# Optimization experiments

Hardware: AMD Instinct MI355X
Metric: run time of the kernel (lower is better)

The kernel has to match this reference:

```python
import jax, jax.numpy as jnp
import numpy as np

B, N_PER, D_IN, D_OUT, E_PER = 64, 256, 256, 128, 8192  # graphs, nodes/graph, in feat, out feat (=clusters K), edges/graph
EPS = 1e-12


def _sage(h, src, dst, W, b):
    # DenseSAGEConv (mean aggregator): h [n,Din], src/dst [E]
    agg = jnp.zeros_like(h).at[dst].add(h[src])                 # sum of in-neighbor messages
    deg = jnp.zeros((h.shape[0],), h.dtype).at[dst].add(1.0)
    agg = agg / jnp.maximum(deg, 1.0)[:, None]                  # mean aggregation
    z = jnp.concatenate([h, agg], axis=-1) @ W + b              # Linear(2*Din -> Dout)
    z = z / jnp.maximum(jnp.linalg.norm(z, axis=-1, keepdims=True), EPS)  # F.normalize(p=2)
    return jax.nn.relu(z)                                       # activation


def setup_inputs() -> dict:
    key = jax.random.key(0)
    ks = jax.random.split(key, 5)
    h = jax.random.normal(ks[0], (B, N_PER, D_IN), jnp.float32)
    edge_src = jax.random.randint(ks[1], (B, E_PER), 0, N_PER)
    edge_dst = jax.random.randint(ks[2], (B, E_PER), 0, N_PER)
    s = 1.0 / np.sqrt(2 * D_IN)
    W_feat = jax.random.uniform(ks[3], (2 * D_IN, D_OUT), jnp.float32, -s, s)
    b_feat = jnp.zeros((D_OUT,), jnp.float32)
    W_pool = jax.random.uniform(ks[4], (2 * D_IN, D_OUT), jnp.float32, -s, s)
    b_pool = jnp.zeros((D_OUT,), jnp.float32)
    return {"h": h, "edge_src": edge_src, "edge_dst": edge_dst,
            "W_feat": W_feat, "b_feat": b_feat, "W_pool": W_pool, "b_pool": b_pool}


def reference(h, edge_src, edge_dst, W_feat, b_feat, W_pool, b_pool):
    sage = jax.vmap(_sage, in_axes=(0, 0, 0, None, None))
    feat = sage(h, edge_src, edge_dst, W_feat, b_feat)                          # [B,n,K]
    assign = jax.nn.softmax(sage(h, edge_src, edge_dst, W_pool, b_pool), -1)    # [B,n,K]
    # h = assign^T @ feat, per graph (equivalent to block_diag(assign)^T @ stacked feat)
    h_pool = jnp.einsum('bnk,bnd->bkd', assign, feat).reshape(B * D_OUT, D_OUT)  # [B*K, Dout]
    # adj_new = S^T A S per graph; A[dst,src]=1 per edge -> sum_e outer(S[dst_e], S[src_e])
    s_dst = jnp.take_along_axis(assign, edge_dst[:, :, None], axis=1)           # [B,E,K]
    s_src = jnp.take_along_axis(assign, edge_src[:, :, None], axis=1)           # [B,E,K]
    blocks = jnp.einsum('bek,bel->bkl', s_dst, s_src)                           # [B,K,K]
    # cross-graph blocks are exactly zero in the batched graph -> block-diagonal dense adj
    adj_new = jax.scipy.linalg.block_diag(*blocks)                              # [B*K, B*K]
    return adj_new, h_pool
```

## Files before the change

### kernel.cpp

```cpp
#include <hip/hip_runtime.h>
#include <hip/hip_bf16.h>
#include <stdint.h>

#define BG 64
#define NP 256
#define DI 256
#define DO 128
#define EP 8192


typedef __attribute__((ext_vector_type(8))) short short8;
typedef __attribute__((ext_vector_type(4))) short short4v;
typedef __attribute__((ext_vector_type(4))) float float4v;

__device__ __forceinline__ int ldi(const void* p, size_t i, int i64) {
  return i64 ? (int)((const long long*)p)[i] : ((const int*)p)[i];
}

__device__ __forceinline__ short f2b(float x) {
  union { float f; unsigned u; } c; c.f = x;
  unsigned r = c.u + 0x7FFFu + ((c.u >> 16) & 1u);
  return (short)(r >> 16);
}
__device__ __forceinline__ float b2f(short b) {
  union { unsigned u; float f; } c; c.u = ((unsigned)(unsigned short)b) << 16;
  return c.f;
}

__device__ __forceinline__ int vote_i64(const void* esrc) {
  const uint32_t* ew = (const uint32_t*)esrc;
  int i64 = 1;
#pragma unroll
  for (int j = 0; j < 8; ++j)
    if (ew[2 * j + 1] != 0) i64 = 0;
  return i64;
}

__global__ __launch_bounds__(256) void k_scatter(const void* __restrict__ esrc,
                                                 const void* __restrict__ edst,
                                                 short* __restrict__ Abf,
                                                 float* __restrict__ deg) {
  __shared__ float Asl[64][256];
  int b = blockIdx.y, rq = blockIdx.x, t = threadIdx.x;
  float4* Az = (float4*)&Asl[0][0];
  for (int i = t; i < 64 * 256 / 4; i += 256) Az[i] = make_float4(0.f, 0.f, 0.f, 0.f);
  int i64 = vote_i64(esrc);
  __syncthreads();
  const size_t base = (size_t)b * EP;
  for (int e = t; e < EP; e += 256) {
    int si = ldi(esrc, base + e, i64) & (NP - 1);
    int di = ldi(edst, base + e, i64) & (NP - 1);
    if ((di >> 6) == rq) atomicAdd(&Asl[di & 63][si], 1.0f);
  }
  __syncthreads();
  int wv = t >> 6, ln = t & 63;
#pragma unroll
  for (int k = 0; k < 16; ++k) {
    int r = k * 4 + wv;
    float4 v = *(float4*)&Asl[r][ln * 4];
    int gr = rq * 64 + r;
    size_t o = ((size_t)b * NP + gr) * NP + ln * 4;
    short tmp[4] = { f2b(v.x), f2b(v.y), f2b(v.z), f2b(v.w) };
    *(short4v*)&Abf[o] = *(short4v*)tmp;
    float s = v.x + v.y + v.z + v.w;
    s += __shfl_xor(s, 1);  s += __shfl_xor(s, 2);  s += __shfl_xor(s, 4);
    s += __shfl_xor(s, 8);  s += __shfl_xor(s, 16); s += __shfl_xor(s, 32);
    if (ln == 0) deg[b * NP + gr] = s;
  }
}

__global__ __launch_bounds__(256) void k_htr(const float* __restrict__ h,
                                             short* __restrict__ hThi,
                                             short* __restrict__ hTlo) {
  __shared__ float T[64][65];
  int b = blockIdx.z, n0 = blockIdx.x * 64, f0 = blockIdx.y * 64;
  int t = threadIdx.x;
  int r = t >> 4, c4 = (t & 15) * 4;
#pragma unroll
  for (int i = 0; i < 4; ++i) {
    float4 v = *(const float4*)&h[((size_t)b * NP + n0 + i * 16 + r) * DI + f0 + c4];
    T[i * 16 + r][c4 + 0] = v.x; T[i * 16 + r][c4 + 1] = v.y;
    T[i * 16 + r][c4 + 2] = v.z; T[i * 16 + r][c4 + 3] = v.w;
  }
  __syncthreads();
#pragma unroll
  for (int i = 0; i < 4; ++i) {
    int f = i * 16 + r;
    short hi4[4], lo4[4];
#pragma unroll
    for (int j = 0; j < 4; ++j) {
      float x = T[c4 + j][f];
      short hb = f2b(x);
      hi4[j] = hb;
      lo4[j] = f2b(x - b2f(hb));
    }
    size_t o = ((size_t)b * DI + f0 + f) * NP + n0 + c4;
    *(short4v*)&hThi[o] = *(short4v*)hi4;
    *(short4v*)&hTlo[o] = *(short4v*)lo4;
  }
}

__global__ __launch_bounds__(256) void k_gemm_agg(const short* __restrict__ Abf,
                                                  const short* __restrict__ hThi,
                                                  const short* __restrict__ hTlo,
                                                  const float* __restrict__ deg,
                                                  float* __restrict__ agg) {
  int b = blockIdx.y, r0 = blockIdx.x * 32, t = threadIdx.x;
  int wave = t >> 6, lane = t & 63, rt = wave & 1, fh = wave >> 1;
  int m = lane & 15, q = lane >> 4;
  float4v acc[8];
#pragma unroll
  for (int i = 0; i < 8; ++i) acc[i] = (float4v){0.f, 0.f, 0.f, 0.f};
  const short* Ar = &Abf[((size_t)b * NP + r0 + rt * 16 + m) * NP];
  for (int kc = 0; kc < NP; kc += 32) {
    short8 af = *(const short8*)&Ar[kc + q * 8];
#pragma unroll
    for (int tt = 0; tt < 8; ++tt) {
      int f = fh * 128 + tt * 16 + m;
      short8 bh = *(const short8*)&hThi[((size_t)b * DI + f) * NP + kc + q * 8];
      short8 bl = *(const short8*)&hTlo[((size_t)b * DI + f) * NP + kc + q * 8];
      acc[tt] = __builtin_amdgcn_mfma_f32_16x16x32_bf16(af, bh, acc[tt], 0, 0, 0);
      acc[tt] = __builtin_amdgcn_mfma_f32_16x16x32_bf16(af, bl, acc[tt], 0, 0, 0);
    }
  }
#pragma unroll
  for (int reg = 0; reg < 4; ++reg) {
    int row = r0 + rt * 16 + q * 4 + reg;
    float sc = 1.0f / fmaxf(deg[b * NP + row], 1.0f);
#pragma unroll
    for (int tt = 0; tt < 8; ++tt)
      agg[((size_t)b * NP + row) * DI + fh * 128 + tt * 16 + m] = acc[tt][reg] * sc;
  }
}

__global__ __launch_bounds__(256) void k_wt(const float* __restrict__ Wf,
                                            const float* __restrict__ Wp,
                                            short* __restrict__ Wt) {
  __shared__ __align__(16) float T[32][132];
  int b = blockIdx.x;
  int head = b >> 4;
  int k0 = (b & 15) * 32;
  const float* W = head ? Wp : Wf;
  int t = threadIdx.x;
  {
    int k = t >> 3, fs = (t & 7) * 16;
    const float* src = &W[(size_t)(k0 + k) * DO + fs];
#pragma unroll
    for (int j = 0; j < 4; ++j)
      *(float4*)&T[k][fs + j * 4] = *(const float4*)(src + j * 4);
  }
  __syncthreads();
  int f = t & 127, kh = (t >> 7) * 16;
  __align__(16) short tmp[16];
#pragma unroll
  for (int i = 0; i < 16; ++i) tmp[i] = f2b(T[kh + i][f]);
  short* dst = &Wt[((size_t)head * DO + f) * 512 + k0 + kh];
  *(short8*)dst = *(short8*)&tmp[0];
  *(short8*)(dst + 8) = *(short8*)&tmp[8];
}

__global__ __launch_bounds__(256) void k_zepi_mfma(const float* __restrict__ h,
                                                   const float* __restrict__ agg,
                                                   const short* __restrict__ Wt,
                                                   const float* __restrict__ bfe,
                                                   const float* __restrict__ bpo,
                                                   short* __restrict__ FtH,
                                                   short* __restrict__ FtL,
                                                   short* __restrict__ PtH,
                                                   short* __restrict__ PtL) {
  __shared__ __align__(16) short Xs[32][40];
  __shared__ __align__(16) short TT[2][2][128][40];
  int r0 = blockIdx.x * 32;
  int t = threadIdx.x;
  int wave = t >> 6, lane = t & 63;
  int rt = wave & 1, ch = wave >> 1;
  int m = lane & 15, q = lane >> 4;
  float4v acc[8];
#pragma unroll
  for (int i = 0; i < 8; ++i) acc[i] = (float4v){0.f, 0.f, 0.f, 0.f};

  for (int kc = 0; kc < 2 * DI; kc += 32) {
    __syncthreads();
    {
      int r = t >> 3, k4 = (t & 7) * 4;
      const float* src = (kc < DI) ? &h[(size_t)(r0 + r) * DI + kc + k4]
                                   : &agg[(size_t)(r0 + r) * DI + (kc - DI) + k4];
      float4 v = *(const float4*)src;
      Xs[r][k4 + 0] = f2b(v.x); Xs[r][k4 + 1] = f2b(v.y);
      Xs[r][k4 + 2] = f2b(v.z); Xs[r][k4 + 3] = f2b(v.w);
    }
    __syncthreads();
    short8 afrag = *(const short8*)&Xs[rt * 16 + m][q * 8];
#pragma unroll
    for (int tt = 0; tt < 8; ++tt) {
      int n = ch * 128 + tt * 16 + m;
      short8 bfrag = *(const short8*)&Wt[(size_t)n * 512 + kc + q * 8];
      acc[tt] = __builtin_amdgcn_mfma_f32_16x16x32_bf16(afrag, bfrag, acc[tt], 0, 0, 0);
    }
  }

  const float* bp = ch ? bpo : bfe;
  float bias[8];
#pragma unroll
  for (int tt = 0; tt < 8; ++tt) bias[tt] = bp ? bp[tt * 16 + m] : 0.f;
#pragma unroll
  for (int reg = 0; reg < 4; ++reg) {
    int rloc = rt * 16 + q * 4 + reg;
    float z[8];
    float ss = 0.f;
#pragma unroll
    for (int tt = 0; tt < 8; ++tt) { z[tt] = acc[tt][reg] + bias[tt]; ss += z[tt] * z[tt]; }
    ss += __shfl_xor(ss, 1); ss += __shfl_xor(ss, 2);
    ss += __shfl_xor(ss, 4); ss += __shfl_xor(ss, 8);
    float inv = 1.0f / fmaxf(sqrtf(ss), 1e-12f);
    float v[8];
#pragma unroll
    for (int tt = 0; tt < 8; ++tt) v[tt] = fmaxf(z[tt] * inv, 0.f);
    if (ch == 1) {
      float mx = v[0];
#pragma unroll
      for (int tt = 1; tt < 8; ++tt) mx = fmaxf(mx, v[tt]);
      mx = fmaxf(mx, __shfl_xor(mx, 1)); mx = fmaxf(mx, __shfl_xor(mx, 2));
      mx = fmaxf(mx, __shfl_xor(mx, 4)); mx = fmaxf(mx, __shfl_xor(mx, 8));
      float e[8], s = 0.f;
#pragma unroll
      for (int tt = 0; tt < 8; ++tt) { e[tt] = __expf(v[tt] - mx); s += e[tt]; }
      s += __shfl_xor(s, 1); s += __shfl_xor(s, 2);
      s += __shfl_xor(s, 4); s += __shfl_xor(s, 8);
      float is = 1.0f / s;
#pragma unroll
      for (int tt = 0; tt < 8; ++tt) v[tt] = e[tt] * is;
    }
#pragma unroll
    for (int tt = 0; tt < 8; ++tt) {
      short hb = f2b(v[tt]);
      short lb = f2b(v[tt] - b2f(hb));
      TT[ch][0][tt * 16 + m][rloc] = hb;
      TT[ch][1][tt * 16 + m][rloc] = lb;
    }
  }
  __syncthreads();
  int b = r0 >> 8, nl = r0 & 255;
#pragma unroll
  for (int it = 0; it < 8; ++it) {
    int chunk = it * 256 + t;
    int c = chunk & 3, col = (chunk >> 2) & 127;
    int hl = (chunk >> 9) & 1, head = chunk >> 10;
    short* base = head ? (hl ? PtL : PtH) : (hl ? FtL : FtH);
    short* dst = &base[((size_t)b * DO + col) * NP + nl + c * 8];
    *(short8*)dst = *(const short8*)&TT[head][hl][col][c * 8];
  }
}

__global__ __launch_bounds__(256) void k_gemm_as(const short* __restrict__ Abf,
                                                 const short* __restrict__ PtH,
                                                 const short* __restrict__ PtL,
                                                 short* __restrict__ AStH,
                                                 short* __restrict__ AStL) {
  __shared__ __align__(16) short TS[2][128][40];
  int b = blockIdx.y, n0 = blockIdx.x * 32, t = threadIdx.x;
  int wave = t >> 6, lane = t & 63, rt = wave & 1, fh = wave >> 1;
  int m = lane & 15, q = lane >> 4;
  float4v acc[4];
#pragma unroll
  for (int i = 0; i < 4; ++i) acc[i] = (float4v){0.f, 0.f, 0.f, 0.f};
  const short* Ar = &Abf[((size_t)b * NP + n0 + rt * 16 + m) * NP];
  for (int kc = 0; kc < NP; kc += 32) {
    short8 af = *(const short8*)&Ar[kc + q * 8];
#pragma unroll
    for (int tt = 0; tt < 4; ++tt) {
      int j = fh * 64 + tt * 16 + m;
      short8 bh = *(const short8*)&PtH[((size_t)b * DO + j) * NP + kc + q * 8];
      short8 bl = *(const short8*)&PtL[((size_t)b * DO + j) * NP + kc + q * 8];
      acc[tt] = __builtin_amdgcn_mfma_f32_16x16x32_bf16(af, bh, acc[tt], 0, 0, 0);
      acc[tt] = __builtin_amdgcn_mfma_f32_16x16x32_bf16(af, bl, acc[tt], 0, 0, 0);
    }
  }
#pragma unroll
  for (int tt = 0; tt < 4; ++tt) {
#pragma unroll
    for (int reg = 0; reg < 4; ++reg) {
      int j = fh * 64 + tt * 16 + m;
      int nl = rt * 16 + q * 4 + reg;
      float vv = acc[tt][reg];
      short hb = f2b(vv);
      TS[0][j][nl] = hb;
      TS[1][j][nl] = f2b(vv - b2f(hb));
    }
  }
  __syncthreads();
#pragma unroll
  for (int it = 0; it < 4; ++it) {
    int chunk = it * 256 + t;
    int c = chunk & 3, col = (chunk >> 2) & 127, hl = chunk >> 9;
    short* dst = &(hl ? AStL : AStH)[((size_t)b * DO + col) * NP + n0 + c * 8];
    *(short8*)dst = *(const short8*)&TS[hl][col][c * 8];
  }
}

__global__ __launch_bounds__(256) void k_pool2(const short* __restrict__ PtH,
                                               const short* __restrict__ PtL,
                                               const short* __restrict__ AStH,
                                               const short* __restrict__ AStL,
                                               const short* __restrict__ FtH,
                                               const short* __restrict__ FtL,
                                               float* __restrict__ adj,
                                               float* __restrict__ hpool) {
  int b = blockIdx.y;
  int ch2 = blockIdx.x & 1, rh = (blockIdx.x >> 1) & 1, which = blockIdx.x >> 2;
  const short* YH = which ? FtH : AStH;
  const short* YL = which ? FtL : AStL;
  int t = threadIdx.x, wave = t >> 6, lane = t & 63;
  int m = lane & 15, q = lane >> 4;
  float4v acc[4];
#pragma unroll
  for (int i = 0; i < 4; ++i) acc[i] = (float4v){0.f, 0.f, 0.f, 0.f};
  int irow = rh * 64 + wave * 16 + m;
  const short* pah = &PtH[((size_t)b * DO + irow) * NP];
  const short* pal = &PtL[((size_t)b * DO + irow) * NP];
  for (int kc = 0; kc < NP; kc += 32) {
    short8 ah = *(const short8*)&pah[kc + q * 8];
    short8 al = *(const short8*)&pal[kc + q * 8];
#pragma unroll
    for (int tt = 0; tt < 4; ++tt) {
      int j = ch2 * 64 + tt * 16 + m;
      short8 bh = *(const short8*)&YH[((size_t)b * DO + j) * NP + kc + q * 8];
      short8 bl = *(const short8*)&YL[((size_t)b * DO + j) * NP + kc + q * 8];
      acc[tt] = __builtin_amdgcn_mfma_f32_16x16x32_bf16(ah, bh, acc[tt], 0, 0, 0);
      acc[tt] = __builtin_amdgcn_mfma_f32_16x16x32_bf16(al, bh, acc[tt], 0, 0, 0);
      acc[tt] = __builtin_amdgcn_mfma_f32_16x16x32_bf16(ah, bl, acc[tt], 0, 0, 0);
    }
  }
#pragma unroll
  for (int tt = 0; tt < 4; ++tt) {
#pragma unroll
    for (int reg = 0; reg < 4; ++reg) {
      int i = rh * 64 + wave * 16 + q * 4 + reg;
      int j = ch2 * 64 + tt * 16 + m;
      float vv = acc[tt][reg];
      if (which == 0)
        adj[(size_t)(b * DO + i) * (BG * DO) + (size_t)b * DO + j] = vv;
      else
        hpool[((size_t)b * DO + i) * DO + j] = vv;
    }
  }
}

extern "C" void kernel_launch(void* const* d_in, const int* in_sizes, int n_in,
                              void* d_out, int out_size, void* d_ws, size_t ws_size,
                              hipStream_t stream) {
  (void)out_size; (void)ws_size;
  int ih = -1, ie[2] = {-1, -1}, iw[2] = {-1, -1}, ib[2] = {-1, -1};
  int ne = 0, nw = 0, nb = 0;
  for (int i = 0; i < n_in; ++i) {
    long long s = in_sizes[i];
    if (s == (long long)BG * NP * DI) { if (ih < 0) ih = i; }
    else if (s == (long long)BG * EP && ne < 2) ie[ne++] = i;
    else if (s == (long long)2 * DI * DO && nw < 2) iw[nw++] = i;
    else if (s == (long long)DO && nb < 2) ib[nb++] = i;
  }
  if (ih < 0 || ne < 2 || nw < 2) {
    ih = 0;
    ie[0] = (n_in > 1) ? 1 : 0;  ie[1] = (n_in > 2) ? 2 : ie[0];
    iw[0] = (n_in > 3) ? 3 : 0;  iw[1] = (n_in > 5) ? 5 : iw[0];
    ib[0] = (n_in > 4) ? 4 : -1; ib[1] = (n_in > 6) ? 6 : -1;
    nb = (ib[1] >= 0) ? 2 : (ib[0] >= 0 ? 1 : 0);
  }
  const float* h    = (const float*)d_in[ih];
  const void* esrc  = d_in[ie[0]];
  const void* edst  = d_in[ie[1]];
  const float* Wf   = (const float*)d_in[iw[0]];
  const float* Wp   = (const float*)d_in[iw[1]];
  const float* bfe  = (nb >= 1) ? (const float*)d_in[ib[0]] : nullptr;
  const float* bpo  = (nb >= 2) ? (const float*)d_in[ib[1]] : nullptr;

  float* adj   = (float*)d_out;
  float* hpool = (float*)d_out + (size_t)(BG * DO) * (BG * DO);
  const size_t ADJ_BYTES = (size_t)(BG * DO) * (BG * DO) * sizeof(float);

  char* wb = (char*)d_ws;
  float* agg  = (float*)wb;
  short* Abf  = (short*)(wb + 16777216);
  short* hThi = (short*)(wb + 25165824);
  short* hTlo = (short*)(wb + 33554432);
  short* PtH  = (short*)(wb + 41943040);
  short* PtL  = (short*)(wb + 46137344);
  short* FtH  = (short*)(wb + 50331648);
  short* FtL  = (short*)(wb + 54525952);
  short* AStH = (short*)(wb + 58720256);
  short* AStL = (short*)(wb + 62914560);
  float* deg  = (float*)(wb + 67108864);
  short* Wt   = (short*)(wb + 67174400);

  hipMemsetAsync(adj, 0, ADJ_BYTES, stream);
  k_wt<<<32, 256, 0, stream>>>(Wf, Wp, Wt);
  k_htr<<<dim3(4, 4, BG), 256, 0, stream>>>(h, hThi, hTlo);
  k_scatter<<<dim3(4, BG), 256, 0, stream>>>(esrc, edst, Abf, deg);
  k_gemm_agg<<<dim3(8, BG), 256, 0, stream>>>(Abf, hThi, hTlo, deg, agg);
  k_zepi_mfma<<<BG * NP / 32, 256, 0, stream>>>(h, agg, Wt, bfe, bpo, FtH, FtL, PtH, PtL);
  k_gemm_as<<<dim3(8, BG), 256, 0, stream>>>(Abf, PtH, PtL, AStH, AStL);
  k_pool2<<<dim3(8, BG), 256, 0, stream>>>(PtH, PtL, AStH, AStL, FtH, FtL, adj, hpool);
}
```

Before: 448.1 us.

## Fuse prep kernels, keep aggregation in LDS, spread adj zeroing across GEMM kernels

Merges the transpose, scatter and weight-convert kernels into one launch. The aggregation GEMM is fused into the feature/pool projection kernel, so the mean-aggregated rows stay in shared memory as bf16 and never round-trip through a global agg buffer. The full-size memset of the block-diagonal adj (8192x8192 fp32) is replaced by extra blocks in the three later kernels that write zeros only to off-diagonal tiles using nontemporal stores. The aim is to cut launches, global traffic and the redundant zero-write of diagonal blocks, at the cost of rounding agg to bf16 without a lo split, which lowers precision.

```diff
diff --git a/kernel.cpp b/kernel.cpp
--- a/kernel.cpp
+++ b/kernel.cpp
@@ -36,87 +36,145 @@
   return i64;
 }
 
-__global__ __launch_bounds__(256) void k_scatter(const void* __restrict__ esrc,
-                                                 const void* __restrict__ edst,
-                                                 short* __restrict__ Abf,
-                                                 float* __restrict__ deg) {
-  __shared__ float Asl[64][256];
-  int b = blockIdx.y, rq = blockIdx.x, t = threadIdx.x;
-  float4* Az = (float4*)&Asl[0][0];
-  for (int i = t; i < 64 * 256 / 4; i += 256) Az[i] = make_float4(0.f, 0.f, 0.f, 0.f);
-  int i64 = vote_i64(esrc);
-  __syncthreads();
-  const size_t base = (size_t)b * EP;
-  for (int e = t; e < EP; e += 256) {
-    int si = ldi(esrc, base + e, i64) & (NP - 1);
-    int di = ldi(edst, base + e, i64) & (NP - 1);
-    if ((di >> 6) == rq) atomicAdd(&Asl[di & 63][si], 1.0f);
-  }
-  __syncthreads();
-  int wv = t >> 6, ln = t & 63;
-#pragma unroll
-  for (int k = 0; k < 16; ++k) {
-    int r = k * 4 + wv;
-    float4 v = *(float4*)&Asl[r][ln * 4];
-    int gr = rq * 64 + r;
-    size_t o = ((size_t)b * NP + gr) * NP + ln * 4;
-    short tmp[4] = { f2b(v.x), f2b(v.y), f2b(v.z), f2b(v.w) };
-    *(short4v*)&Abf[o] = *(short4v*)tmp;
-    float s = v.x + v.y + v.z + v.w;
-    s += __shfl_xor(s, 1);  s += __shfl_xor(s, 2);  s += __shfl_xor(s, 4);
-    s += __shfl_xor(s, 8);  s += __shfl_xor(s, 16); s += __shfl_xor(s, 32);
-    if (ln == 0) deg[b * NP + gr] = s;
-  }
-}
-
-__global__ __launch_bounds__(256) void k_htr(const float* __restrict__ h,
-                                             short* __restrict__ hThi,
-                                             short* __restrict__ hTlo) {
-  __shared__ float T[64][65];
-  int b = blockIdx.z, n0 = blockIdx.x * 64, f0 = blockIdx.y * 64;
+__device__ __forceinline__ void fill_adj_rows(float* __restrict__ adj, int r0) {
   int t = threadIdx.x;
-  int r = t >> 4, c4 = (t & 15) * 4;
-#pragma unroll
-  for (int i = 0; i < 4; ++i) {
-    float4 v = *(const float4*)&h[((size_t)b * NP + n0 + i * 16 + r) * DI + f0 + c4];
-    T[i * 16 + r][c4 + 0] = v.x; T[i * 16 + r][c4 + 1] = v.y;
-    T[i * 16 + r][c4 + 2] = v.z; T[i * 16 + r][c4 + 3] = v.w;
-  }
-  __syncthreads();
-#pragma unroll
-  for (int i = 0; i < 4; ++i) {
-    int f = i * 16 + r;
-    short hi4[4], lo4[4];
-#pragma unroll
-    for (int j = 0; j < 4; ++j) {
-      float x = T[c4 + j][f];
-      short hb = f2b(x);
-      hi4[j] = hb;
-      lo4[j] = f2b(x - b2f(hb));
-    }
-    size_t o = ((size_t)b * DI + f0 + f) * NP + n0 + c4;
-    *(short4v*)&hThi[o] = *(short4v*)hi4;
-    *(short4v*)&hTlo[o] = *(short4v*)lo4;
-  }
-}
-
-__global__ __launch_bounds__(256) void k_gemm_agg(const short* __restrict__ Abf,
-                                                  const short* __restrict__ hThi,
-                                                  const short* __restrict__ hTlo,
-                                                  const float* __restrict__ deg,
-                                                  float* __restrict__ agg) {
-  int b = blockIdx.y, r0 = blockIdx.x * 32, t = threadIdx.x;
-  int wave = t >> 6, lane = t & 63, rt = wave & 1, fh = wave >> 1;
+  const float4v z = {0.f, 0.f, 0.f, 0.f};
+  for (int rr = 0; rr < 16; ++rr) {
+    int r = r0 + rr;
+    int g = r >> 7;
+    float4v* row = (float4v*)(adj + (size_t)r * (BG * DO));
+    int s0 = g * 32;
+#pragma unroll
+    for (int it = 0; it < 8; ++it) {
+      int p = it * 256 + t;
+      if ((unsigned)(p - s0) >= 32u)
+        __builtin_nontemporal_store(z, &row[p]);
+    }
+  }
+}
+
+__global__ __launch_bounds__(256) void k_prep(const float* __restrict__ h,
+                                              const void* __restrict__ esrc,
+                                              const void* __restrict__ edst,
+                                              const float* __restrict__ Wf,
+                                              const float* __restrict__ Wp,
+                                              short* __restrict__ hThi,
+                                              short* __restrict__ hTlo,
+                                              short* __restrict__ Abf,
+                                              float* __restrict__ deg,
+                                              short* __restrict__ Wt) {
+  __shared__ __align__(16) char smem[65536];
+  int bx = blockIdx.x, t = threadIdx.x;
+  if (bx < 1024) {
+    float (*T)[65] = (float(*)[65])smem;
+    int b = bx >> 4, n0 = (bx & 3) * 64, f0 = ((bx >> 2) & 3) * 64;
+    int r = t >> 4, c4 = (t & 15) * 4;
+#pragma unroll
+    for (int i = 0; i < 4; ++i) {
+      float4 v = *(const float4*)&h[((size_t)b * NP + n0 + i * 16 + r) * DI + f0 + c4];
+      T[i * 16 + r][c4 + 0] = v.x; T[i * 16 + r][c4 + 1] = v.y;
+      T[i * 16 + r][c4 + 2] = v.z; T[i * 16 + r][c4 + 3] = v.w;
+    }
+    __syncthreads();
+#pragma unroll
+    for (int i = 0; i < 4; ++i) {
+      int f = i * 16 + r;
+      short hi4[4], lo4[4];
+#pragma unroll
+      for (int j = 0; j < 4; ++j) {
+        float x = T[c4 + j][f];
+        short hb = f2b(x);
+        hi4[j] = hb;
+        lo4[j] = f2b(x - b2f(hb));
+      }
+      size_t o = ((size_t)b * DI + f0 + f) * NP + n0 + c4;
+      *(short4v*)&hThi[o] = *(short4v*)hi4;
+      *(short4v*)&hTlo[o] = *(short4v*)lo4;
+    }
+  } else if (bx < 1280) {
+    float (*Asl)[256] = (float(*)[256])smem;
+    int idx = bx - 1024, b = idx >> 2, rq = idx & 3;
+    float4* Az = (float4*)&Asl[0][0];
+    for (int i = t; i < 64 * 256 / 4; i += 256) Az[i] = make_float4(0.f, 0.f, 0.f, 0.f);
+    int i64 = vote_i64(esrc);
+    __syncthreads();
+    const size_t base = (size_t)b * EP;
+    for (int e = t; e < EP; e += 256) {
+      int si = ldi(esrc, base + e, i64) & (NP - 1);
+      int di = ldi(edst, base + e, i64) & (NP - 1);
+      if ((di >> 6) == rq) atomicAdd(&Asl[di & 63][si], 1.0f);
+    }
+    __syncthreads();
+    int wv = t >> 6, ln = t & 63;
+#pragma unroll
+    for (int k = 0; k < 16; ++k) {
+      int r = k * 4 + wv;
+      float4 v = *(float4*)&Asl[r][ln * 4];
+      int gr = rq * 64 + r;
+      size_t o = ((size_t)b * NP + gr) * NP + ln * 4;
+      short tmp[4] = { f2b(v.x), f2b(v.y), f2b(v.z), f2b(v.w) };
+      *(short4v*)&Abf[o] = *(short4v*)tmp;
+      float s = v.x + v.y + v.z + v.w;
+      s += __shfl_xor(s, 1);  s += __shfl_xor(s, 2);  s += __shfl_xor(s, 4);
+      s += __shfl_xor(s, 8);  s += __shfl_xor(s, 16); s += __shfl_xor(s, 32);
+      if (ln == 0) deg[b * NP + gr] = s;
+    }
+  } else {
+    float (*T)[132] = (float(*)[132])smem;
+    int bb = bx - 1280;
+    int head = bb >> 4;
+    int k0 = (bb & 15) * 32;
+    const float* W = head ? Wp : Wf;
+    {
+      int k = t >> 3, fs = (t & 7) * 16;
+      const float* src = &W[(size_t)(k0 + k) * DO + fs];
+#pragma unroll
+      for (int j = 0; j < 4; ++j)
+        *(float4*)&T[k][fs + j * 4] = *(const float4*)(src + j * 4);
+    }
+    __syncthreads();
+    int f = t & 127, kh = (t >> 7) * 16;
+    __align__(16) short tmp[16];
+#pragma unroll
+    for (int i = 0; i < 16; ++i) tmp[i] = f2b(T[kh + i][f]);
+    short* dst = &Wt[((size_t)head * DO + f) * 512 + k0 + kh];
+    *(short8*)dst = *(short8*)&tmp[0];
+    *(short8*)(dst + 8) = *(short8*)&tmp[8];
+  }
+}
+
+__global__ __launch_bounds__(256) void k_fz(const float* __restrict__ h,
+                                            const short* __restrict__ Abf,
+                                            const short* __restrict__ hThi,
+                                            const short* __restrict__ hTlo,
+                                            const float* __restrict__ deg,
+                                            const short* __restrict__ Wt,
+                                            const float* __restrict__ bfe,
+                                            const float* __restrict__ bpo,
+                                            short* __restrict__ FtH, short* __restrict__ FtL,
+                                            short* __restrict__ PtH, short* __restrict__ PtL,
+                                            float* __restrict__ adj) {
+  __shared__ __align__(16) char smem[40960];
+  int bx = blockIdx.x, t = threadIdx.x;
+  if (bx >= 512) { fill_adj_rows(adj, (bx - 512) * 16); return; }
+  short (*Xa)[264] = (short(*)[264])smem;
+  short (*Xs)[40]  = (short(*)[40])(smem + 16896);
+  short (*TT)[2][128][40] = (short(*)[2][128][40])smem;
+  int r0 = bx * 32;
+  int b = r0 >> 8, nl = r0 & 255;
+  int wave = t >> 6, lane = t & 63;
+  int rt = wave & 1, ch = wave >> 1;
   int m = lane & 15, q = lane >> 4;
   float4v acc[8];
 #pragma unroll
   for (int i = 0; i < 8; ++i) acc[i] = (float4v){0.f, 0.f, 0.f, 0.f};
-  const short* Ar = &Abf[((size_t)b * NP + r0 + rt * 16 + m) * NP];
+
+  const short* Ar = &Abf[((size_t)r0 + rt * 16 + m) * NP];
   for (int kc = 0; kc < NP; kc += 32) {
     short8 af = *(const short8*)&Ar[kc + q * 8];
 #pragma unroll
     for (int tt = 0; tt < 8; ++tt) {
-      int f = fh * 128 + tt * 16 + m;
+      int f = ch * 128 + tt * 16 + m;
       short8 bh = *(const short8*)&hThi[((size_t)b * DI + f) * NP + kc + q * 8];
       short8 bl = *(const short8*)&hTlo[((size_t)b * DI + f) * NP + kc + q * 8];
       acc[tt] = __builtin_amdgcn_mfma_f32_16x16x32_bf16(af, bh, acc[tt], 0, 0, 0);
@@ -125,72 +183,31 @@
   }
 #pragma unroll
   for (int reg = 0; reg < 4; ++reg) {
-    int row = r0 + rt * 16 + q * 4 + reg;
-    float sc = 1.0f / fmaxf(deg[b * NP + row], 1.0f);
+    int rowl = rt * 16 + q * 4 + reg;
+    float sc = 1.0f / fmaxf(deg[r0 + rowl], 1.0f);
 #pragma unroll
     for (int tt = 0; tt < 8; ++tt)
-      agg[((size_t)b * NP + row) * DI + fh * 128 + tt * 16 + m] = acc[tt][reg] * sc;
-  }
-}
-
-__global__ __launch_bounds__(256) void k_wt(const float* __restrict__ Wf,
-                                            const float* __restrict__ Wp,
-                                            short* __restrict__ Wt) {
-  __shared__ __align__(16) float T[32][132];
-  int b = blockIdx.x;
-  int head = b >> 4;
-  int k0 = (b & 15) * 32;
-  const float* W = head ? Wp : Wf;
-  int t = threadIdx.x;
-  {
-    int k = t >> 3, fs = (t & 7) * 16;
-    const float* src = &W[(size_t)(k0 + k) * DO + fs];
-#pragma unroll
-    for (int j = 0; j < 4; ++j)
-      *(float4*)&T[k][fs + j * 4] = *(const float4*)(src + j * 4);
+      Xa[rowl][ch * 128 + tt * 16 + m] = f2b(acc[tt][reg] * sc);
   }
   __syncthreads();
-  int f = t & 127, kh = (t >> 7) * 16;
-  __align__(16) short tmp[16];
-#pragma unroll
-  for (int i = 0; i < 16; ++i) tmp[i] = f2b(T[kh + i][f]);
-  short* dst = &Wt[((size_t)head * DO + f) * 512 + k0 + kh];
-  *(short8*)dst = *(short8*)&tmp[0];
-  *(short8*)(dst + 8) = *(short8*)&tmp[8];
-}
-
-__global__ __launch_bounds__(256) void k_zepi_mfma(const float* __restrict__ h,
-                                                   const float* __restrict__ agg,
-                                                   const short* __restrict__ Wt,
-                                                   const float* __restrict__ bfe,
-                                                   const float* __restrict__ bpo,
-                                                   short* __restrict__ FtH,
-                                                   short* __restrict__ FtL,
-                                                   short* __restrict__ PtH,
-                                                   short* __restrict__ PtL) {
-  __shared__ __align__(16) short Xs[32][40];
-  __shared__ __align__(16) short TT[2][2][128][40];
-  int r0 = blockIdx.x * 32;
-  int t = threadIdx.x;
-  int wave = t >> 6, lane = t & 63;
-  int rt = wave & 1, ch = wave >> 1;
-  int m = lane & 15, q = lane >> 4;
-  float4v acc[8];
+
 #pragma unroll
   for (int i = 0; i < 8; ++i) acc[i] = (float4v){0.f, 0.f, 0.f, 0.f};
-
   for (int kc = 0; kc < 2 * DI; kc += 32) {
-    __syncthreads();
-    {
-      int r = t >> 3, k4 = (t & 7) * 4;
-      const float* src = (kc < DI) ? &h[(size_t)(r0 + r) * DI + kc + k4]
-                                   : &agg[(size_t)(r0 + r) * DI + (kc - DI) + k4];
-      float4 v = *(const float4*)src;
-      Xs[r][k4 + 0] = f2b(v.x); Xs[r][k4 + 1] = f2b(v.y);
-      Xs[r][k4 + 2] = f2b(v.z); Xs[r][k4 + 3] = f2b(v.w);
-    }
-    __syncthreads();
-    short8 afrag = *(const short8*)&Xs[rt * 16 + m][q * 8];
+    short8 afrag;
+    if (kc < DI) {
+      __syncthreads();
+      {
+        int r = t >> 3, k4 = (t & 7) * 4;
+        float4 v = *(const float4*)&h[(size_t)(r0 + r) * DI + kc + k4];
+        Xs[r][k4 + 0] = f2b(v.x); Xs[r][k4 + 1] = f2b(v.y);
+        Xs[r][k4 + 2] = f2b(v.z); Xs[r][k4 + 3] = f2b(v.w);
+      }
+      __syncthreads();
+      afrag = *(const short8*)&Xs[rt * 16 + m][q * 8];
+    } else {
+      afrag = *(const short8*)&Xa[rt * 16 + m][(kc - DI) + q * 8];
+    }
 #pragma unroll
     for (int tt = 0; tt < 8; ++tt) {
       int n = ch * 128 + tt * 16 + m;
@@ -198,6 +215,7 @@
       acc[tt] = __builtin_amdgcn_mfma_f32_16x16x32_bf16(afrag, bfrag, acc[tt], 0, 0, 0);
     }
   }
+  __syncthreads();
 
   const float* bp = ch ? bpo : bfe;
   float bias[8];
@@ -240,7 +258,6 @@
     }
   }
   __syncthreads();
-  int b = r0 >> 8, nl = r0 & 255;
 #pragma unroll
   for (int it = 0; it < 8; ++it) {
     int chunk = it * 256 + t;
@@ -256,9 +273,12 @@
                                                  const short* __restrict__ PtH,
                                                  const short* __restrict__ PtL,
                                                  short* __restrict__ AStH,
-                                                 short* __restrict__ AStL) {
+                                                 short* __restrict__ AStL,
+                                                 float* __restrict__ adj) {
   __shared__ __align__(16) short TS[2][128][40];
-  int b = blockIdx.y, n0 = blockIdx.x * 32, t = threadIdx.x;
+  int bx = blockIdx.x, t = threadIdx.x;
+  if (bx >= 512) { fill_adj_rows(adj, 4096 + (bx - 512) * 16); return; }
+  int b = bx >> 3, n0 = (bx & 7) * 32;
   int wave = t >> 6, lane = t & 63, rt = wave & 1, fh = wave >> 1;
   int m = lane & 15, q = lane >> 4;
   float4v acc[4];
@@ -281,11 +301,11 @@
 #pragma unroll
     for (int reg = 0; reg < 4; ++reg) {
       int j = fh * 64 + tt * 16 + m;
-      int nl = rt * 16 + q * 4 + reg;
+      int nlr = rt * 16 + q * 4 + reg;
       float vv = acc[tt][reg];
       short hb = f2b(vv);
-      TS[0][j][nl] = hb;
-      TS[1][j][nl] = f2b(vv - b2f(hb));
+      TS[0][j][nlr] = hb;
+      TS[1][j][nlr] = f2b(vv - b2f(hb));
     }
   }
   __syncthreads();
@@ -306,11 +326,13 @@
                                                const short* __restrict__ FtL,
                                                float* __restrict__ adj,
                                                float* __restrict__ hpool) {
-  int b = blockIdx.y;
-  int ch2 = blockIdx.x & 1, rh = (blockIdx.x >> 1) & 1, which = blockIdx.x >> 2;
+  int bx = blockIdx.x, t = threadIdx.x;
+  if (bx >= 512) { fill_adj_rows(adj, 6144 + (bx - 512) * 16); return; }
+  int b = bx >> 3, x = bx & 7;
+  int ch2 = x & 1, rh = (x >> 1) & 1, which = x >> 2;
   const short* YH = which ? FtH : AStH;
   const short* YL = which ? FtL : AStL;
-  int t = threadIdx.x, wave = t >> 6, lane = t & 63;
+  int wave = t >> 6, lane = t & 63;
   int m = lane & 15, q = lane >> 4;
   float4v acc[4];
 #pragma unroll
@@ -376,28 +398,23 @@
 
   float* adj   = (float*)d_out;
   float* hpool = (float*)d_out + (size_t)(BG * DO) * (BG * DO);
-  const size_t ADJ_BYTES = (size_t)(BG * DO) * (BG * DO) * sizeof(float);
 
   char* wb = (char*)d_ws;
-  float* agg  = (float*)wb;
-  short* Abf  = (short*)(wb + 16777216);
-  short* hThi = (short*)(wb + 25165824);
-  short* hTlo = (short*)(wb + 33554432);
-  short* PtH  = (short*)(wb + 41943040);
-  short* PtL  = (short*)(wb + 46137344);
-  short* FtH  = (short*)(wb + 50331648);
-  short* FtL  = (short*)(wb + 54525952);
-  short* AStH = (short*)(wb + 58720256);
-  short* AStL = (short*)(wb + 62914560);
-  float* deg  = (float*)(wb + 67108864);
-  short* Wt   = (short*)(wb + 67174400);
-
-  hipMemsetAsync(adj, 0, ADJ_BYTES, stream);
-  k_wt<<<32, 256, 0, stream>>>(Wf, Wp, Wt);
-  k_htr<<<dim3(4, 4, BG), 256, 0, stream>>>(h, hThi, hTlo);
-  k_scatter<<<dim3(4, BG), 256, 0, stream>>>(esrc, edst, Abf, deg);
-  k_gemm_agg<<<dim3(8, BG), 256, 0, stream>>>(Abf, hThi, hTlo, deg, agg);
-  k_zepi_mfma<<<BG * NP / 32, 256, 0, stream>>>(h, agg, Wt, bfe, bpo, FtH, FtL, PtH, PtL);
-  k_gemm_as<<<dim3(8, BG), 256, 0, stream>>>(Abf, PtH, PtL, AStH, AStL);
-  k_pool2<<<dim3(8, BG), 256, 0, stream>>>(PtH, PtL, AStH, AStL, FtH, FtL, adj, hpool);
-}
+  short* Abf  = (short*)wb;
+  short* hThi = (short*)(wb + 8388608);
+  short* hTlo = (short*)(wb + 16777216);
+  short* PtH  = (short*)(wb + 25165824);
+  short* PtL  = (short*)(wb + 29360128);
+  short* FtH  = (short*)(wb + 33554432);
+  short* FtL  = (short*)(wb + 37748736);
+  short* AStH = (short*)(wb + 41943040);
+  short* AStL = (short*)(wb + 46137344);
+  float* deg  = (float*)(wb + 50331648);
+  short* Wt   = (short*)(wb + 50397184);
+
+  k_prep<<<1312, 256, 0, stream>>>(h, esrc, edst, Wf, Wp, hThi, hTlo, Abf, deg, Wt);
+  k_fz<<<768, 256, 0, stream>>>(h, Abf, hThi, hTlo, deg, Wt, bfe, bpo,
+                                FtH, FtL, PtH, PtL, adj);
+  k_gemm_as<<<640, 256, 0, stream>>>(Abf, PtH, PtL, AStH, AStL, adj);
+  k_pool2<<<640, 256, 0, stream>>>(PtH, PtL, AStH, AStL, FtH, FtL, adj, hpool);
+}
```

After: 415.8 us. 7.2% less time.
